# Performance work log

Measured on AMD Instinct MI355X. Metric: run time of the kernel, lower is better.

Reference implementation:

```python
import jax, jax.numpy as jnp
import numpy as np

B, A, D = 512, 32, 256      # batch clips, actors (nodes per graph), feature dim
E = 1048576                 # total edges over the flattened (B*A)-node graph
THRESHOLD = 0.5             # config.knn.threshold
EPS = 1e-5


def setup_inputs() -> dict:
    key = jax.random.key(0)
    k1, k2, k3 = jax.random.split(key, 3)
    N = B * A
    X = jax.random.normal(k1, (B, A, D), dtype=jnp.float32)
    edge_index = jax.random.randint(k2, (2, E), 0, N, dtype=jnp.int32)
    W = jax.random.normal(k3, (D, D), dtype=jnp.float32) * (1.0 / np.sqrt(D))
    b = jnp.zeros((D,), dtype=jnp.float32)
    return {"X": X, "edge_index": edge_index, "W": W, "b": b}


def gcn_conv(x, edge_index, W, b):
    # Standard GCNConv: x' = D^-1/2 (A + I) D^-1/2 (x W) + b
    N = x.shape[0]
    x = x @ W                                            # [N, D]
    loop = jnp.arange(N, dtype=edge_index.dtype)
    src = jnp.concatenate([edge_index[0], loop])         # message sources
    tgt = jnp.concatenate([edge_index[1], loop])         # aggregation targets
    deg = jax.ops.segment_sum(jnp.ones_like(src, dtype=x.dtype), tgt,
                              num_segments=N)            # in-degree incl. self-loop
    dinv = jnp.where(deg > 0, jax.lax.rsqrt(deg), 0.0)
    coef = (dinv[src] * dinv[tgt])[:, None]              # symmetric norm per edge
    out = jax.ops.segment_sum(x[src] * coef, tgt, num_segments=N)
    return out + b


def reference(X, edge_index, W, b):
    Bq, Aq, Dq = X.shape
    x = X.reshape(Bq * Aq, Dq)
    x = gcn_conv(x, edge_index, W, b)
    Xo = x.reshape(Bq, Aq, Dq)

    # cal_edge: pairwise squared distances per batch, min-max normalized,
    # thresholded. Instead of variable-length dense_to_sparse edge lists we
    # return the equivalent fixed-shape adjacency mask [B, A, A].
    inner = -2.0 * jnp.einsum('bad,bcd->bac', Xo, Xo)
    sq = jnp.sum(Xo * Xo, axis=-1, keepdims=True)        # [B, A, 1]
    scores = sq + inner + jnp.swapaxes(sq, -1, -2)       # [B, A, A]
    smin = scores.min(axis=-1, keepdims=True)
    smax = scores.max(axis=-1, keepdims=True)
    scores = (scores - smin) / (smax - smin + EPS)
    adj_mask = scores > THRESHOLD                        # new edge set (dense form)
    return Xo, adj_mask
```

## Files before the change

kernel.cpp:

```cpp
#include <hip/hip_runtime.h>

#define BQ 512
#define AQ 32
#define DQ 256
#define NQ (BQ * AQ)
#define EQ 1048576
#define THR 0.5f
#define EPSF 1e-5f
#define DEG_STRIDE 160
#define BIN_TGTS 64
#define NBINS (NQ / BIN_TGTS)
#define BIN_STRIDE 4864

typedef __attribute__((ext_vector_type(8))) short bf16x8;
typedef __attribute__((ext_vector_type(4))) float f32x4;

__device__ __forceinline__ unsigned short f2bf(float f) {
    unsigned int u = __float_as_uint(f);
    return (unsigned short)((u + 0x7FFFu + ((u >> 16) & 1u)) >> 16);
}
__device__ __forceinline__ float bf2f(unsigned short h) {
    return __uint_as_float((unsigned int)h << 16);
}

__global__ __launch_bounds__(256) void k_wt(
        const float* __restrict__ W, unsigned short* __restrict__ Wt,
        int* __restrict__ bin_cursor) {
    int tid = threadIdx.x;
    int idx = blockIdx.x * 256 + tid;
    int n = idx >> 8;
    int k = idx & 255;
    float w = W[k * DQ + n];
    unsigned short h = f2bf(w);
    Wt[idx] = h;
    Wt[DQ * DQ + idx] = f2bf(w - bf2f(h));
    if (blockIdx.x == 0) bin_cursor[tid] = 0;
}

__global__ __launch_bounds__(256) void k_part_gemm(
        const float* __restrict__ Xp, const unsigned short* __restrict__ Wt,
        unsigned short* __restrict__ xwb,
        const int* __restrict__ src, const int* __restrict__ tgt,
        int* __restrict__ bin_cursor, unsigned int* __restrict__ binned) {
    __shared__ int hist[NBINS];
    int tid = threadIdx.x;
    if (blockIdx.x < 256) {
        hist[tid] = 0;
        __syncthreads();
        int base = blockIdx.x * 4096;
        int t[16], s[16];
        #pragma unroll
        for (int i = 0; i < 16; i++) {
            int e = base + i * 256 + tid;
            t[i] = tgt[e];
            s[i] = src[e];
            atomicAdd(&hist[t[i] >> 6], 1);
        }
        __syncthreads();
        int mine = hist[tid];
        __syncthreads();
        hist[tid] = tid * BIN_STRIDE + atomicAdd(&bin_cursor[tid], mine);
        __syncthreads();
        #pragma unroll
        for (int i = 0; i < 16; i++) {
            int slot = atomicAdd(&hist[t[i] >> 6], 1);
            binned[slot] = ((unsigned int)t[i] << 14) | (unsigned int)s[i];
        }
        return;
    }
    int wave = tid >> 6;
    int lane = tid & 63;
    int col = lane & 15;
    int quad = lane >> 4;
    int mbase = (blockIdx.x - 256) * 64 + wave * 16;
    int m = mbase + col;

    const float* arow = Xp + (size_t)m * DQ;
    const unsigned short* Wlo = Wt + DQ * DQ;

    f32x4 acc[16];
    f32x4 zero = {0.f, 0.f, 0.f, 0.f};
    #pragma unroll
    for (int i = 0; i < 16; i++) acc[i] = zero;

    for (int k0 = 0; k0 < DQ; k0 += 32) {
        int kq = k0 + quad * 8;
        float4 a0 = *(const float4*)(arow + kq);
        float4 a1 = *(const float4*)(arow + kq + 4);
        float av[8] = {a0.x, a0.y, a0.z, a0.w, a1.x, a1.y, a1.z, a1.w};
        bf16x8 ah, al;
        #pragma unroll
        for (int j = 0; j < 8; j++) {
            unsigned short h = f2bf(av[j]);
            ah[j] = (short)h;
            al[j] = (short)f2bf(av[j] - bf2f(h));
        }
        #pragma unroll
        for (int nt = 0; nt < 16; nt++) {
            size_t boff = (size_t)(nt * 16 + col) * DQ + kq;
            bf16x8 bh = *(const bf16x8*)(Wt + boff);
            bf16x8 bl = *(const bf16x8*)(Wlo + boff);
            acc[nt] = __builtin_amdgcn_mfma_f32_16x16x32_bf16(ah, bh, acc[nt], 0, 0, 0);
            acc[nt] = __builtin_amdgcn_mfma_f32_16x16x32_bf16(al, bh, acc[nt], 0, 0, 0);
            acc[nt] = __builtin_amdgcn_mfma_f32_16x16x32_bf16(ah, bl, acc[nt], 0, 0, 0);
        }
    }

    #pragma unroll
    for (int nt = 0; nt < 16; nt++) {
        #pragma unroll
        for (int r = 0; r < 4; r++) {
            xwb[(size_t)(mbase + quad * 4 + r) * DQ + nt * 16 + col] =
                f2bf(acc[nt][r]);
        }
    }
}

__global__ __launch_bounds__(256) void k_cnt(
        const int* __restrict__ bin_cursor, const unsigned int* __restrict__ binned,
        float* __restrict__ dinv) {
    __shared__ int lcnt[BIN_TGTS];
    int tid = threadIdx.x;
    int b = blockIdx.x;
    if (tid < BIN_TGTS) lcnt[tid] = 0;
    __syncthreads();
    int beg = b * BIN_STRIDE;
    int count = bin_cursor[b];
    if (count > BIN_STRIDE) count = BIN_STRIDE;
    for (int i = beg + tid; i < beg + count; i += 256) {
        unsigned int ed = binned[i];
        atomicAdd(&lcnt[(ed >> 14) & 63], 1);
    }
    __syncthreads();
    if (tid < BIN_TGTS)
        dinv[b * BIN_TGTS + tid] = rsqrtf((float)(lcnt[tid] + 1));
}

__global__ __launch_bounds__(512) void k_agg_scores(
        const unsigned int* __restrict__ xwb,
        const unsigned int* __restrict__ binned,
        const int* __restrict__ bin_cursor,
        const float* __restrict__ dinv,
        const float* __restrict__ bias,
        float* __restrict__ out,
        float* __restrict__ mask) {
    __shared__ float xs[AQ][DQ + 4];
    __shared__ float sq[AQ];
    __shared__ float sc[AQ][AQ + 1];
    __shared__ float rmin[AQ], rmax[AQ];
    __shared__ unsigned short lbuck[AQ * DEG_STRIDE];
    __shared__ int lcnt[AQ];

    int tid = threadIdx.x;
    int wave = tid >> 6;
    int lane = tid & 63;
    int bq = blockIdx.x;
    const uint2* xw2 = (const uint2*)xwb;

    if (tid < AQ) lcnt[tid] = 0;
    __syncthreads();
    {
        int b = bq >> 1;
        int beg = b * BIN_STRIDE;
        int count = bin_cursor[b];
        if (count > BIN_STRIDE) count = BIN_STRIDE;
        for (int i = beg + tid; i < beg + count; i += 512) {
            unsigned int ed = binned[i];
            if ((int)(ed >> 19) == bq) {
                int a = (ed >> 14) & 31;
                int pos = atomicAdd(&lcnt[a], 1);
                if (pos < DEG_STRIDE)
                    lbuck[a * DEG_STRIDE + pos] = (unsigned short)(ed & 0x3FFFu);
            }
        }
    }
    __syncthreads();

    float4 bv = ((const float4*)bias)[lane];

    #pragma unroll 1
    for (int i = 0; i < 4; i++) {
        int a = wave * 4 + i;
        int t = bq * AQ + a;
        float dt = dinv[t];
        float c0 = dt * dt;
        uint2 sp = xw2[(size_t)t * 64 + lane];
        float4 acc;
        acc.x = __uint_as_float(sp.x << 16) * c0;
        acc.y = __uint_as_float(sp.x & 0xFFFF0000u) * c0;
        acc.z = __uint_as_float(sp.y << 16) * c0;
        acc.w = __uint_as_float(sp.y & 0xFFFF0000u) * c0;

        int num = lcnt[a];
        if (num > DEG_STRIDE) num = DEG_STRIDE;
        for (int k0 = 0; k0 < num; k0 += 64) {
            int rem = num - k0;
            int n = rem < 64 ? rem : 64;
            int idx = k0 + (lane < n ? lane : 0);
            int e = (int)lbuck[a * DEG_STRIDE + idx];
            float cl = (lane < n) ? dinv[e] * dt : 0.f;
            int n8 = (n + 7) & ~7;
            for (int j0 = 0; j0 < n8; j0 += 8) {
                #pragma unroll
                for (int jj = 0; jj < 8; jj++) {
                    int j = j0 + jj;
                    int s = __shfl(e, j);
                    float c = __shfl(cl, j);
                    uint2 p = xw2[(size_t)s * 64 + lane];
                    acc.x += __uint_as_float(p.x << 16) * c;
                    acc.y += __uint_as_float(p.x & 0xFFFF0000u) * c;
                    acc.z += __uint_as_float(p.y << 16) * c;
                    acc.w += __uint_as_float(p.y & 0xFFFF0000u) * c;
                }
            }
        }

        acc.x += bv.x; acc.y += bv.y; acc.z += bv.z; acc.w += bv.w;
        ((float4*)out)[(size_t)t * 64 + lane] = acc;
        *(float4*)&xs[a][lane * 4] = acc;
    }
    __syncthreads();

    if (tid < AQ) {
        const float4* xi = (const float4*)xs[tid];
        float s = 0.f;
        #pragma unroll 8
        for (int dd = 0; dd < DQ / 4; dd++) {
            float4 a = xi[dd];
            s += a.x * a.x + a.y * a.y + a.z * a.z + a.w * a.w;
        }
        sq[tid] = s;
    }
    __syncthreads();

    {
        int p0 = tid * 2;
        int i = p0 >> 5;
        int j0 = p0 & 31;
        const float4* xi = (const float4*)xs[i];
        float g[2] = {0.f, 0.f};
        for (int dd = 0; dd < DQ / 4; dd += 8) {
            float4 ar[8];
            #pragma unroll
            for (int u = 0; u < 8; u++) ar[u] = xi[dd + u];
            #pragma unroll
            for (int q = 0; q < 2; q++) {
                const float4* xj = (const float4*)xs[j0 + q];
                float gq = 0.f;
                #pragma unroll
                for (int u = 0; u < 8; u++) {
                    float4 b = xj[dd + u];
                    gq += ar[u].x * b.x + ar[u].y * b.y +
                          ar[u].z * b.z + ar[u].w * b.w;
                }
                g[q] += gq;
            }
        }
        #pragma unroll
        for (int q = 0; q < 2; q++) {
            sc[i][j0 + q] = sq[i] - 2.f * g[q] + sq[j0 + q];
        }
    }
    __syncthreads();

    if (tid < AQ) {
        float mn = sc[tid][0], mx = sc[tid][0];
        for (int j = 1; j < AQ; j++) {
            float v = sc[tid][j];
            mn = fminf(mn, v);
            mx = fmaxf(mx, v);
        }
        rmin[tid] = mn;
        rmax[tid] = mx;
    }
    __syncthreads();

    {
        float* mb = mask + (size_t)bq * AQ * AQ;
        int p0 = tid * 2;
        int i = p0 >> 5, j0 = p0 & 31;
        float inv = 1.0f / (rmax[i] - rmin[i] + EPSF);
        float2 mv;
        mv.x = ((sc[i][j0 + 0] - rmin[i]) * inv > THR) ? 1.0f : 0.0f;
        mv.y = ((sc[i][j0 + 1] - rmin[i]) * inv > THR) ? 1.0f : 0.0f;
        ((float2*)mb)[tid] = mv;
    }
}

extern "C" void kernel_launch(void* const* d_in, const int* in_sizes, int n_in,
                              void* d_out, int out_size, void* d_ws, size_t ws_size,
                              hipStream_t stream) {
    const float* X    = (const float*)d_in[0];
    const int*   ei   = (const int*)d_in[1];
    const float* W    = (const float*)d_in[2];
    const float* bias = (const float*)d_in[3];
    float* out = (float*)d_out;

    char* ws = (char*)d_ws;
    unsigned short* xwb = (unsigned short*)ws;
    unsigned int* binned = (unsigned int*)(ws + (size_t)NQ * DQ * 2);
    unsigned short* Wt = (unsigned short*)(binned + (size_t)NBINS * BIN_STRIDE);
    float* dinv = (float*)(Wt + 2 * DQ * DQ);
    int* bin_cursor = (int*)(dinv + NQ);

    const int* src = ei;
    const int* tgt = ei + EQ;

    k_wt<<<256, 256, 0, stream>>>(W, Wt, bin_cursor);
    k_part_gemm<<<512, 256, 0, stream>>>(X, Wt, xwb, src, tgt, bin_cursor, binned);
    k_cnt<<<256, 256, 0, stream>>>(bin_cursor, binned, dinv);
    k_agg_scores<<<BQ, 512, 0, stream>>>((const unsigned int*)xwb, binned,
                                         bin_cursor, dinv, bias, out,
                                         out + (size_t)NQ * DQ);
}
```

Measured before the change: 188.0 us.

## Fold degree counting into partition kernel and prefetch next edge chunk

Removes the separate k_cnt kernel. In-degrees are now counted with global atomics during the partition pass, and rsqrt is computed on the fly in the aggregation kernel. The aggregation loop also prefetches the next 64-edge chunk's indices and coefficients while processing the current one, and unrolls the gather 16-wide. This saves one launch and one pass over the binned edges, at the cost of about a million global atomics and a repeated rsqrt per edge.

```diff
diff --git a/kernel.cpp b/kernel.cpp
--- a/kernel.cpp
+++ b/kernel.cpp
@@ -25,7 +25,7 @@
 
 __global__ __launch_bounds__(256) void k_wt(
         const float* __restrict__ W, unsigned short* __restrict__ Wt,
-        int* __restrict__ bin_cursor) {
+        int* __restrict__ bin_cursor, int* __restrict__ deg) {
     int tid = threadIdx.x;
     int idx = blockIdx.x * 256 + tid;
     int n = idx >> 8;
@@ -34,6 +34,7 @@
     unsigned short h = f2bf(w);
     Wt[idx] = h;
     Wt[DQ * DQ + idx] = f2bf(w - bf2f(h));
+    if (tid < 64) deg[blockIdx.x * 64 + tid] = 0;
     if (blockIdx.x == 0) bin_cursor[tid] = 0;
 }
 
@@ -41,7 +42,8 @@
         const float* __restrict__ Xp, const unsigned short* __restrict__ Wt,
         unsigned short* __restrict__ xwb,
         const int* __restrict__ src, const int* __restrict__ tgt,
-        int* __restrict__ bin_cursor, unsigned int* __restrict__ binned) {
+        int* __restrict__ bin_cursor, unsigned int* __restrict__ binned,
+        int* __restrict__ deg) {
     __shared__ int hist[NBINS];
     int tid = threadIdx.x;
     if (blockIdx.x < 256) {
@@ -66,6 +68,8 @@
             int slot = atomicAdd(&hist[t[i] >> 6], 1);
             binned[slot] = ((unsigned int)t[i] << 14) | (unsigned int)s[i];
         }
+        #pragma unroll
+        for (int i = 0; i < 16; i++) atomicAdd(&deg[t[i]], 1);
         return;
     }
     int wave = tid >> 6;
@@ -116,31 +120,11 @@
     }
 }
 
-__global__ __launch_bounds__(256) void k_cnt(
-        const int* __restrict__ bin_cursor, const unsigned int* __restrict__ binned,
-        float* __restrict__ dinv) {
-    __shared__ int lcnt[BIN_TGTS];
-    int tid = threadIdx.x;
-    int b = blockIdx.x;
-    if (tid < BIN_TGTS) lcnt[tid] = 0;
-    __syncthreads();
-    int beg = b * BIN_STRIDE;
-    int count = bin_cursor[b];
-    if (count > BIN_STRIDE) count = BIN_STRIDE;
-    for (int i = beg + tid; i < beg + count; i += 256) {
-        unsigned int ed = binned[i];
-        atomicAdd(&lcnt[(ed >> 14) & 63], 1);
-    }
-    __syncthreads();
-    if (tid < BIN_TGTS)
-        dinv[b * BIN_TGTS + tid] = rsqrtf((float)(lcnt[tid] + 1));
-}
-
 __global__ __launch_bounds__(512) void k_agg_scores(
         const unsigned int* __restrict__ xwb,
         const unsigned int* __restrict__ binned,
         const int* __restrict__ bin_cursor,
-        const float* __restrict__ dinv,
+        const int* __restrict__ deg,
         const float* __restrict__ bias,
         float* __restrict__ out,
         float* __restrict__ mask) {
@@ -182,7 +166,7 @@
     for (int i = 0; i < 4; i++) {
         int a = wave * 4 + i;
         int t = bq * AQ + a;
-        float dt = dinv[t];
+        float dt = rsqrtf((float)(deg[t] + 1));
         float c0 = dt * dt;
         uint2 sp = xw2[(size_t)t * 64 + lane];
         float4 acc;
@@ -193,19 +177,33 @@
 
         int num = lcnt[a];
         if (num > DEG_STRIDE) num = DEG_STRIDE;
+
+        int e_cur = 0, n_cur = 0;
+        float cl_cur = 0.f;
+        if (num > 0) {
+            n_cur = num < 64 ? num : 64;
+            int idx = (lane < n_cur ? lane : 0);
+            e_cur = (int)lbuck[a * DEG_STRIDE + idx];
+            cl_cur = (lane < n_cur) ? rsqrtf((float)(deg[e_cur] + 1)) * dt : 0.f;
+        }
+        #pragma unroll 1
         for (int k0 = 0; k0 < num; k0 += 64) {
-            int rem = num - k0;
-            int n = rem < 64 ? rem : 64;
-            int idx = k0 + (lane < n ? lane : 0);
-            int e = (int)lbuck[a * DEG_STRIDE + idx];
-            float cl = (lane < n) ? dinv[e] * dt : 0.f;
-            int n8 = (n + 7) & ~7;
-            for (int j0 = 0; j0 < n8; j0 += 8) {
+            int k1 = k0 + 64;
+            int e_nxt = 0, n_nxt = 0;
+            float cl_nxt = 0.f;
+            if (k1 < num) {
+                n_nxt = (num - k1) < 64 ? (num - k1) : 64;
+                int idx = k1 + (lane < n_nxt ? lane : 0);
+                e_nxt = (int)lbuck[a * DEG_STRIDE + idx];
+                cl_nxt = (lane < n_nxt) ? rsqrtf((float)(deg[e_nxt] + 1)) * dt : 0.f;
+            }
+            int n16 = (n_cur + 15) & ~15;
+            for (int j0 = 0; j0 < n16; j0 += 16) {
                 #pragma unroll
-                for (int jj = 0; jj < 8; jj++) {
+                for (int jj = 0; jj < 16; jj++) {
                     int j = j0 + jj;
-                    int s = __shfl(e, j);
-                    float c = __shfl(cl, j);
+                    int s = __shfl(e_cur, j);
+                    float c = __shfl(cl_cur, j);
                     uint2 p = xw2[(size_t)s * 64 + lane];
                     acc.x += __uint_as_float(p.x << 16) * c;
                     acc.y += __uint_as_float(p.x & 0xFFFF0000u) * c;
@@ -213,6 +211,7 @@
                     acc.w += __uint_as_float(p.y & 0xFFFF0000u) * c;
                 }
             }
+            e_cur = e_nxt; cl_cur = cl_nxt; n_cur = n_nxt;
         }
 
         acc.x += bv.x; acc.y += bv.y; acc.z += bv.z; acc.w += bv.w;
@@ -300,16 +299,16 @@
     unsigned short* xwb = (unsigned short*)ws;
     unsigned int* binned = (unsigned int*)(ws + (size_t)NQ * DQ * 2);
     unsigned short* Wt = (unsigned short*)(binned + (size_t)NBINS * BIN_STRIDE);
-    float* dinv = (float*)(Wt + 2 * DQ * DQ);
-    int* bin_cursor = (int*)(dinv + NQ);
+    int* deg = (int*)(Wt + 2 * DQ * DQ);
+    int* bin_cursor = (int*)(deg + NQ);
 
     const int* src = ei;
     const int* tgt = ei + EQ;
 
-    k_wt<<<256, 256, 0, stream>>>(W, Wt, bin_cursor);
-    k_part_gemm<<<512, 256, 0, stream>>>(X, Wt, xwb, src, tgt, bin_cursor, binned);
-    k_cnt<<<256, 256, 0, stream>>>(bin_cursor, binned, dinv);
+    k_wt<<<256, 256, 0, stream>>>(W, Wt, bin_cursor, deg);
+    k_part_gemm<<<512, 256, 0, stream>>>(X, Wt, xwb, src, tgt, bin_cursor,
+                                         binned, deg);
     k_agg_scores<<<BQ, 512, 0, stream>>>((const unsigned int*)xwb, binned,
-                                         bin_cursor, dinv, bias, out,
+                                         bin_cursor, deg, bias, out,
                                          out + (size_t)NQ * DQ);
 }
```

Result: slower. 216.9 us (+15.4%).

## Split partition and GEMM kernels; stage W tiles in shared memory

Applied to the files above, without the earlier changes.

The fused partition+GEMM kernel is split into two separate launches. The GEMM now cooperatively loads each 32-wide K slice of the hi and lo bf16 W planes into padded LDS, and all four waves read it from there instead of each fetching W from global/L2. This cuts redundant global traffic for W. In exchange it adds two barriers per K step and one extra kernel launch, and the partition work no longer overlaps with the GEMM.

```diff
diff --git a/kernel.cpp b/kernel.cpp
--- a/kernel.cpp
+++ b/kernel.cpp
@@ -37,42 +37,44 @@
     if (blockIdx.x == 0) bin_cursor[tid] = 0;
 }
 
-__global__ __launch_bounds__(256) void k_part_gemm(
-        const float* __restrict__ Xp, const unsigned short* __restrict__ Wt,
-        unsigned short* __restrict__ xwb,
+__global__ __launch_bounds__(256) void k_part(
         const int* __restrict__ src, const int* __restrict__ tgt,
         int* __restrict__ bin_cursor, unsigned int* __restrict__ binned) {
     __shared__ int hist[NBINS];
     int tid = threadIdx.x;
-    if (blockIdx.x < 256) {
-        hist[tid] = 0;
-        __syncthreads();
-        int base = blockIdx.x * 4096;
-        int t[16], s[16];
-        #pragma unroll
-        for (int i = 0; i < 16; i++) {
-            int e = base + i * 256 + tid;
-            t[i] = tgt[e];
-            s[i] = src[e];
-            atomicAdd(&hist[t[i] >> 6], 1);
-        }
-        __syncthreads();
-        int mine = hist[tid];
-        __syncthreads();
-        hist[tid] = tid * BIN_STRIDE + atomicAdd(&bin_cursor[tid], mine);
-        __syncthreads();
-        #pragma unroll
-        for (int i = 0; i < 16; i++) {
-            int slot = atomicAdd(&hist[t[i] >> 6], 1);
-            binned[slot] = ((unsigned int)t[i] << 14) | (unsigned int)s[i];
-        }
-        return;
-    }
+    hist[tid] = 0;
+    __syncthreads();
+    int base = blockIdx.x * 4096;
+    int t[16], s[16];
+    #pragma unroll
+    for (int i = 0; i < 16; i++) {
+        int e = base + i * 256 + tid;
+        t[i] = tgt[e];
+        s[i] = src[e];
+        atomicAdd(&hist[t[i] >> 6], 1);
+    }
+    __syncthreads();
+    int mine = hist[tid];
+    __syncthreads();
+    hist[tid] = tid * BIN_STRIDE + atomicAdd(&bin_cursor[tid], mine);
+    __syncthreads();
+    #pragma unroll
+    for (int i = 0; i < 16; i++) {
+        int slot = atomicAdd(&hist[t[i] >> 6], 1);
+        binned[slot] = ((unsigned int)t[i] << 14) | (unsigned int)s[i];
+    }
+}
+
+__global__ __launch_bounds__(256) void k_gemm(
+        const float* __restrict__ Xp, const unsigned short* __restrict__ Wt,
+        unsigned short* __restrict__ xwb) {
+    __shared__ unsigned short bs[2][256 * 40];
+    int tid = threadIdx.x;
     int wave = tid >> 6;
     int lane = tid & 63;
     int col = lane & 15;
     int quad = lane >> 4;
-    int mbase = (blockIdx.x - 256) * 64 + wave * 16;
+    int mbase = blockIdx.x * 64 + wave * 16;
     int m = mbase + col;
 
     const float* arow = Xp + (size_t)m * DQ;
@@ -84,6 +86,19 @@
     for (int i = 0; i < 16; i++) acc[i] = zero;
 
     for (int k0 = 0; k0 < DQ; k0 += 32) {
+        __syncthreads();
+        {
+            const uint4* gh = (const uint4*)(Wt + tid * DQ + k0);
+            const uint4* gl = (const uint4*)(Wlo + tid * DQ + k0);
+            uint4* lh = (uint4*)&bs[0][tid * 40];
+            uint4* ll = (uint4*)&bs[1][tid * 40];
+            #pragma unroll
+            for (int u = 0; u < 4; u++) lh[u] = gh[u];
+            #pragma unroll
+            for (int u = 0; u < 4; u++) ll[u] = gl[u];
+        }
+        __syncthreads();
+
         int kq = k0 + quad * 8;
         float4 a0 = *(const float4*)(arow + kq);
         float4 a1 = *(const float4*)(arow + kq + 4);
@@ -97,9 +112,9 @@
         }
         #pragma unroll
         for (int nt = 0; nt < 16; nt++) {
-            size_t boff = (size_t)(nt * 16 + col) * DQ + kq;
-            bf16x8 bh = *(const bf16x8*)(Wt + boff);
-            bf16x8 bl = *(const bf16x8*)(Wlo + boff);
+            int n = nt * 16 + col;
+            bf16x8 bh = *(const bf16x8*)&bs[0][n * 40 + quad * 8];
+            bf16x8 bl = *(const bf16x8*)&bs[1][n * 40 + quad * 8];
             acc[nt] = __builtin_amdgcn_mfma_f32_16x16x32_bf16(ah, bh, acc[nt], 0, 0, 0);
             acc[nt] = __builtin_amdgcn_mfma_f32_16x16x32_bf16(al, bh, acc[nt], 0, 0, 0);
             acc[nt] = __builtin_amdgcn_mfma_f32_16x16x32_bf16(ah, bl, acc[nt], 0, 0, 0);
@@ -307,7 +322,8 @@
     const int* tgt = ei + EQ;
 
     k_wt<<<256, 256, 0, stream>>>(W, Wt, bin_cursor);
-    k_part_gemm<<<512, 256, 0, stream>>>(X, Wt, xwb, src, tgt, bin_cursor, binned);
+    k_part<<<256, 256, 0, stream>>>(src, tgt, bin_cursor, binned);
+    k_gemm<<<256, 256, 0, stream>>>(X, Wt, xwb);
     k_cnt<<<256, 256, 0, stream>>>(bin_cursor, binned, dinv);
     k_agg_scores<<<BQ, 512, 0, stream>>>((const unsigned int*)xwb, binned,
                                          bin_cursor, dinv, bias, out,
```

Result: faster. 179.1 us (-4.7%).
